# Kernel optimization log

Hardware: AMD Instinct MI355X
Metric: run time of the kernel (lower is better)

## Reference

```python
import jax, jax.numpy as jnp
import numpy as np

B, L, D, E, F, K = 2, 1024, 768, 16, 3072, 2


def setup_inputs() -> dict:
    key = jax.random.key(0)
    ks = jax.random.split(key, 6)
    s = 0.02  # GPT-style init scale
    x = jax.random.normal(ks[0], (B, L, D), dtype=jnp.float32)
    wr = jax.random.normal(ks[1], (E, D), dtype=jnp.float32) * s   # router.weight [out,in]
    w1 = jax.random.normal(ks[2], (E, F, D), dtype=jnp.float32) * s  # expert fc1 weights
    b1 = jnp.zeros((E, F), dtype=jnp.float32)
    w2 = jax.random.normal(ks[3], (E, D, F), dtype=jnp.float32) * s  # expert fc2 weights
    b2 = jnp.zeros((E, D), dtype=jnp.float32)
    return {"x": x, "wr": wr, "w1": w1, "b1": b1, "w2": w2, "b2": b2}


def reference(x, wr, w1, b1, w2, b2):
    # --- router: softmax over experts, top-k gate built by scatter ---
    logits = jnp.einsum("bld,ed->ble", x, wr)            # [B,L,E]
    probs = jax.nn.softmax(logits, axis=-1)
    top_p, ix = jax.lax.top_k(probs, K)                   # [B,L,K]
    # gate[b,l,e] = top_p where e in ix else 0  (scatter_ equivalent)
    gate = jnp.sum(jax.nn.one_hot(ix, E, dtype=x.dtype) * top_p[..., None], axis=-2)  # [B,L,E]
    # --- dense: every expert over every token (matches original loop) ---
    h = jnp.einsum("bld,efd->blef", x, w1) + b1           # [B,L,E,F]
    h = jax.nn.gelu(h, approximate=False)                 # torch nn.GELU (exact erf)
    y = jnp.einsum("blef,edf->bled", h, w2) + b2          # [B,L,E,D]
    out = x + jnp.einsum("bled,ble->bld", y, gate)        # gated combine + residual
    return out
```

## Files before the change

kernel.cpp:

```cpp
#include <hip/hip_runtime.h>


#define D_      768
#define E_      16
#define F_      3072
#define NTOK    2048
#define NROWS   4096
#define SEG     384
#define MAXROWS 6144
#define BK      64
#define BNW     192

typedef __attribute__((ext_vector_type(2))) unsigned int   u32x2;
typedef __attribute__((ext_vector_type(4))) unsigned int   u32x4;
typedef __attribute__((ext_vector_type(8))) unsigned short u16x8;
typedef __attribute__((ext_vector_type(8))) short          v8bf;
typedef __attribute__((ext_vector_type(4))) float          f32x4;

static __device__ inline unsigned short f2bf(float f) {
    unsigned u = __builtin_bit_cast(unsigned, f);
    u += 0x7fffu + ((u >> 16) & 1u);
    return (unsigned short)(u >> 16);
}
static __device__ __forceinline__ unsigned cvt_pk_bf16(float lo, float hi) {
    unsigned r;
    asm("v_cvt_pk_bf16_f32 %0, %1, %2" : "=v"(r) : "v"(lo), "v"(hi));
    return r;
}

__global__ void router_kernel(const float* __restrict__ x, const float* __restrict__ wr,
                              int* __restrict__ idx, float* __restrict__ gate) {
    const int tok  = blockIdx.x;
    const int lane = threadIdx.x;
    const float* xr = x + (size_t)tok * D_;

    float xv[12];
#pragma unroll
    for (int j = 0; j < 12; ++j) xv[j] = xr[lane + 64 * j];

    float lg[E_];
#pragma unroll
    for (int e = 0; e < E_; ++e) {
        const float* w = wr + (size_t)e * D_;
        float acc = 0.f;
#pragma unroll
        for (int j = 0; j < 12; ++j) acc += xv[j] * w[lane + 64 * j];
#pragma unroll
        for (int s = 32; s > 0; s >>= 1) acc += __shfl_xor(acc, s, 64);
        lg[e] = acc;
    }

    float m = lg[0];
#pragma unroll
    for (int e = 1; e < E_; ++e) m = fmaxf(m, lg[e]);
    float p[E_], s = 0.f;
#pragma unroll
    for (int e = 0; e < E_; ++e) { p[e] = expf(lg[e] - m); s += p[e]; }
    const float inv = 1.f / s;

    int e0 = 0; float p0 = p[0];
#pragma unroll
    for (int e = 1; e < E_; ++e) if (p[e] > p0) { p0 = p[e]; e0 = e; }
    int e1 = -1; float p1 = -1.f;
#pragma unroll
    for (int e = 0; e < E_; ++e) if (e != e0 && p[e] > p1) { p1 = p[e]; e1 = e; }

    if (lane == 0) {
        idx[tok * 2 + 0] = e0;  gate[tok * 2 + 0] = p0 * inv;
        idx[tok * 2 + 1] = e1;  gate[tok * 2 + 1] = p1 * inv;
    }
}

__global__ void build_kernel(const int* __restrict__ idx, const float* __restrict__ gate,
                             int* __restrict__ rowmap, float* __restrict__ rowgate,
                             int* __restrict__ posOf) {
    __shared__ int cur[E_];
    const int t = threadIdx.x;
    if (t < E_) cur[t] = 0;
    __syncthreads();
    for (int i = t; i < MAXROWS; i += 256) { rowmap[i] = 0; rowgate[i] = 0.f; }
    __syncthreads();
    for (int i = t; i < NROWS; i += 256) {
        const int e = idx[i];
        const int o = atomicAdd(&cur[e], 1);
        if (o < SEG) {
            const int pos = e * SEG + o;
            rowmap[pos]  = i >> 1;
            rowgate[pos] = gate[i];
            posOf[i]     = pos;
        } else {
            posOf[i] = e * SEG;
        }
    }
}

__global__ void gather_kernel(const float* __restrict__ x, const int* __restrict__ rowmap,
                              unsigned short* __restrict__ Xg) {
    const int g = blockIdx.x * 256 + threadIdx.x;
    const int pos = g / (D_ / 8), c = g % (D_ / 8);
    const int tok = rowmap[pos];
    const float* src = x + (size_t)tok * D_ + c * 8;
    f32x4 a = *(const f32x4*)src;
    f32x4 b = *(const f32x4*)(src + 4);
    u16x8 o;
    o[0] = f2bf(a[0]); o[1] = f2bf(a[1]); o[2] = f2bf(a[2]); o[3] = f2bf(a[3]);
    o[4] = f2bf(b[0]); o[5] = f2bf(b[1]); o[6] = f2bf(b[2]); o[7] = f2bf(b[3]);
    *(u16x8*)(Xg + (size_t)pos * D_ + c * 8) = o;
}

template <int EPI, int NNSH, int KLEN>
__global__ __launch_bounds__(1024, 4)
void gemm_kernel(const unsigned short* __restrict__ Ag, const float* __restrict__ Bw,
                 const float* __restrict__ bias, unsigned short* __restrict__ C0,
                 unsigned short* __restrict__ C123, const float* __restrict__ rowgate,
                 const int K, const int N) {
    constexpr int NT = KLEN / BK;

    const int bid   = blockIdx.x;
    const int e     = bid & 15;
    const int rest  = bid >> 4;
    const int n     = rest & ((1 << NNSH) - 1);
    const int split = rest >> NNSH;
    const int m0    = e * SEG;
    const int n0    = n * BNW;
    const int kOff  = split * KLEN;

    __shared__ alignas(16) unsigned short As[2][SEG * BK];
    __shared__ alignas(16) unsigned short Bs[2][BNW * BK];

    const int t    = threadIdx.x;
    const int lane = t & 63;
    const int wv   = t >> 6;
    const int wm   = wv >> 2;
    const int wn   = wv & 3;
    const int r16  = lane & 15;
    const int h    = lane >> 4;
    const int xorL = (r16 & 7) << 4;

    f32x4 acc[6][3];
#pragma unroll
    for (int i = 0; i < 6; ++i)
#pragma unroll
        for (int j = 0; j < 3; ++j) acc[i][j] = (f32x4){0.f, 0.f, 0.f, 0.f};

    unsigned aByte[3];  int aPhys[3];
#pragma unroll
    for (int i = 0; i < 3; ++i) {
        const int c = t + 1024 * i, r = c >> 3, s = c & 7;
        aByte[i] = (unsigned)(((m0 + r) * K + kOff + s * 8) * 2);
        aPhys[i] = r * 64 + ((s ^ (r & 7)) * 8);
    }
    unsigned bByte[3];  int bOff[3];
#pragma unroll
    for (int i = 0; i < 3; ++i) {
        const int sB = t + 1024 * i, r = sB >> 4, c = sB & 15;
        bByte[i] = (unsigned)((((e * N) + n0 + r) * (size_t)K + kOff + c * 4) * 4);
        bOff[i]  = r * 64 + ((((c >> 1) ^ (r & 7))) << 3) + (c & 1) * 4;
    }

    u32x4 areg[3];
    f32x4 breg[3];

    auto loadA = [&](int kt) {
#pragma unroll
        for (int i = 0; i < 3; ++i)
            areg[i] = *(const u32x4*)((const char*)Ag + aByte[i] + kt * (BK * 2));
    };
    auto loadB = [&](int kt) {
#pragma unroll
        for (int i = 0; i < 3; ++i)
            breg[i] = *(const f32x4*)((const char*)Bw + bByte[i] + kt * (BK * 4));
    };
    auto writeA = [&](int buf) {
#pragma unroll
        for (int i = 0; i < 3; ++i)
            *(u32x4*)&As[buf][aPhys[i]] = areg[i];
    };
    auto writeB = [&](int buf) {
#pragma unroll
        for (int i = 0; i < 3; ++i) {
            u32x2 q;
            q[0] = cvt_pk_bf16(breg[i][0], breg[i][1]);
            q[1] = cvt_pk_bf16(breg[i][2], breg[i][3]);
            *(u32x2*)&Bs[buf][bOff[i]] = q;
        }
    };
    auto compute = [&](int buf) {
#pragma unroll
        for (int ks = 0; ks < 2; ++ks) {
            const int co = ((ks * 64 + h * 16) ^ xorL) >> 1;
            v8bf bfr[3];
#pragma unroll
            for (int nf = 0; nf < 3; ++nf)
                bfr[nf] = *(const v8bf*)&Bs[buf][(wn * 48 + nf * 16 + r16) * 64 + co];
#pragma unroll
            for (int mf = 0; mf < 6; ++mf) {
                const v8bf af = *(const v8bf*)&As[buf][(wm * 96 + mf * 16 + r16) * 64 + co];
#pragma unroll
                for (int nf = 0; nf < 3; ++nf)
                    acc[mf][nf] = __builtin_amdgcn_mfma_f32_16x16x32_bf16(
                        af, bfr[nf], acc[mf][nf], 0, 0, 0);
            }
        }
    };

    loadA(0); loadB(0);
    writeB(0); writeA(0);
    __syncthreads();

    int cb = 0;
    for (int kt = 0; kt < NT; ++kt) {
        if (kt + 1 < NT) { loadB(kt + 1); loadA(kt + 1); }
        compute(cb);
        if (kt + 1 < NT) { writeB(cb ^ 1); writeA(cb ^ 1); }
        __syncthreads();
        cb ^= 1;
    }

    unsigned short* myC = (EPI == 0 || split == 0)
                        ? C0 : C123 + (size_t)(split - 1) * MAXROWS * N;
#pragma unroll
    for (int mf = 0; mf < 6; ++mf) {
#pragma unroll
        for (int jj = 0; jj < 4; ++jj) {
            const int rr = m0 + wm * 96 + mf * 16 + h * 4 + jj;
            float gt = 0.f;
            if (EPI == 1) gt = rowgate[rr];
#pragma unroll
            for (int nf = 0; nf < 3; ++nf) {
                const int cc = n0 + wn * 48 + nf * 16 + r16;
                float v = acc[mf][nf][jj];
                if (EPI == 0) {
                    v += bias[e * N + cc];
                    const float ge = 0.5f * v * (1.f + erff(v * 0.70710678118654752f));
                    myC[(size_t)rr * N + cc] = f2bf(ge);
                } else {
                    if (split == 0) v += bias[e * N + cc];
                    myC[(size_t)rr * N + cc] = f2bf(v * gt);
                }
            }
        }
    }
}

__global__ void combine_kernel(const float* __restrict__ x,
                               const unsigned short* __restrict__ Yp0,
                               const unsigned short* __restrict__ Yp123,
                               const int* __restrict__ posOf, float* __restrict__ out,
                               const int nsplit) {
    const int tok = blockIdx.x;
    const int t   = threadIdx.x;
    const int p0 = posOf[tok * 2 + 0];
    const int p1 = posOf[tok * 2 + 1];
    f32x4 v = *(const f32x4*)(x + (size_t)tok * D_ + t * 4);
    for (int s = 0; s < nsplit; ++s) {
        const unsigned short* base = (s == 0) ? Yp0
                                   : Yp123 + (size_t)(s - 1) * MAXROWS * D_;
        const unsigned short* a = base + (size_t)p0 * D_ + t * 4;
        const unsigned short* b = base + (size_t)p1 * D_ + t * 4;
#pragma unroll
        for (int i = 0; i < 4; ++i) {
            v[i] += __builtin_bit_cast(float, (unsigned)a[i] << 16);
            v[i] += __builtin_bit_cast(float, (unsigned)b[i] << 16);
        }
    }
    *(f32x4*)(out + (size_t)tok * D_ + t * 4) = v;
}

extern "C" void kernel_launch(void* const* d_in, const int* in_sizes, int n_in,
                              void* d_out, int out_size, void* d_ws, size_t ws_size,
                              hipStream_t stream) {
    const float* x  = (const float*)d_in[0];
    const float* wr = (const float*)d_in[1];
    const float* w1 = (const float*)d_in[2];
    const float* b1 = (const float*)d_in[3];
    const float* w2 = (const float*)d_in[4];
    const float* b2 = (const float*)d_in[5];
    float* out = (float*)d_out;

    char* wsp = (char*)d_ws;
    int*            idxP    = (int*)(wsp + 0);
    float*          gateP   = (float*)(wsp + 16384);
    int*            posOf   = (int*)(wsp + 32768);
    int*            rowmap  = (int*)(wsp + 49152);
    float*          rowgate = (float*)(wsp + 73728);
    const size_t    XG_OFF  = 131072;
    const size_t    PLANE   = (size_t)MAXROWS * D_ * 2;
    const size_t    H_OFF   = XG_OFF + PLANE;
    const size_t    H_BYTES = (size_t)MAXROWS * F_ * 2;
    unsigned short* Xg    = (unsigned short*)(wsp + XG_OFF);
    unsigned short* H     = (unsigned short*)(wsp + H_OFF);
    unsigned short* Yp0   = Xg;
    unsigned short* Yp123 = (unsigned short*)(wsp + H_OFF + H_BYTES);

    const bool split4 = (ws_size >= H_OFF + H_BYTES + 3 * PLANE);

    router_kernel<<<NTOK, 64, 0, stream>>>(x, wr, idxP, gateP);
    build_kernel<<<1, 256, 0, stream>>>(idxP, gateP, rowmap, rowgate, posOf);
    gather_kernel<<<MAXROWS * (D_ / 8) / 256, 256, 0, stream>>>(x, rowmap, Xg);

    gemm_kernel<0, 4, 768><<<E_ * 16, 1024, 0, stream>>>(
        Xg, w1, b1, H, (unsigned short*)nullptr, rowgate, D_, F_);

    if (split4) {
        gemm_kernel<1, 2, 768><<<E_ * 16, 1024, 0, stream>>>(
            H, w2, b2, Yp0, Yp123, rowgate, F_, D_);
        combine_kernel<<<NTOK, 192, 0, stream>>>(x, Yp0, Yp123, posOf, out, 4);
    } else {
        gemm_kernel<1, 2, 3072><<<E_ * 4, 1024, 0, stream>>>(
            H, w2, b2, Yp0, Yp123, rowgate, F_, D_);
        combine_kernel<<<NTOK, 192, 0, stream>>>(x, Yp0, Yp123, posOf, out, 1);
    }
}
```

Before: 159.2 us.

## Shrink GEMM tiles and skip MFMA work for unused expert row slabs

Halves the GEMM tile width and K-step, reduces blocks to 512 threads (8 waves), and doubles grid size so more workgroups run concurrently. The build kernel now records per-expert token counts, and waves whose 96-row slab lies beyond the expert's valid rows skip MFMA compute and the epilogue. This aims to avoid wasted matrix work on padded rows of the 384-row expert segments and to improve occupancy, at the cost of more global weight re-reads and more loop iterations with barriers.

```diff
diff --git a/kernel.cpp b/kernel.cpp
--- a/kernel.cpp
+++ b/kernel.cpp
@@ -8,8 +8,8 @@
 #define NROWS   4096
 #define SEG     384
 #define MAXROWS 6144
-#define BK      64
-#define BNW     192
+#define BK      32
+#define BNW     96
 
 typedef __attribute__((ext_vector_type(2))) unsigned int   u32x2;
 typedef __attribute__((ext_vector_type(4))) unsigned int   u32x4;
@@ -73,7 +73,7 @@
 
 __global__ void build_kernel(const int* __restrict__ idx, const float* __restrict__ gate,
                              int* __restrict__ rowmap, float* __restrict__ rowgate,
-                             int* __restrict__ posOf) {
+                             int* __restrict__ posOf, int* __restrict__ meta) {
     __shared__ int cur[E_];
     const int t = threadIdx.x;
     if (t < E_) cur[t] = 0;
@@ -92,6 +92,8 @@
             posOf[i] = e * SEG;
         }
     }
+    __syncthreads();
+    if (t < E_) meta[t] = cur[t] < SEG ? cur[t] : SEG;
 }
 
 __global__ void gather_kernel(const float* __restrict__ x, const int* __restrict__ rowmap,
@@ -109,11 +111,11 @@
 }
 
 template <int EPI, int NNSH, int KLEN>
-__global__ __launch_bounds__(1024, 4)
+__global__ __launch_bounds__(512, 4)
 void gemm_kernel(const unsigned short* __restrict__ Ag, const float* __restrict__ Bw,
                  const float* __restrict__ bias, unsigned short* __restrict__ C0,
                  unsigned short* __restrict__ C123, const float* __restrict__ rowgate,
-                 const int K, const int N) {
+                 const int* __restrict__ meta, const int K, const int N) {
     constexpr int NT = KLEN / BK;
 
     const int bid   = blockIdx.x;
@@ -131,11 +133,14 @@
     const int t    = threadIdx.x;
     const int lane = t & 63;
     const int wv   = t >> 6;
-    const int wm   = wv >> 2;
-    const int wn   = wv & 3;
+    const int wm   = wv >> 1;
+    const int wn   = wv & 1;
     const int r16  = lane & 15;
     const int h    = lane >> 4;
-    const int xorL = (r16 & 7) << 4;
+    const int co   = ((h ^ ((r16 >> 1) & 3)) * 8);
+
+    const int  cnt = meta[e];
+    const bool act = (wm * 96) < cnt;
 
     f32x4 acc[6][3];
 #pragma unroll
@@ -146,20 +151,22 @@
     unsigned aByte[3];  int aPhys[3];
 #pragma unroll
     for (int i = 0; i < 3; ++i) {
-        const int c = t + 1024 * i, r = c >> 3, s = c & 7;
+        const int c = t + 512 * i, r = c >> 2, s = c & 3;
         aByte[i] = (unsigned)(((m0 + r) * K + kOff + s * 8) * 2);
-        aPhys[i] = r * 64 + ((s ^ (r & 7)) * 8);
-    }
-    unsigned bByte[3];  int bOff[3];
-#pragma unroll
-    for (int i = 0; i < 3; ++i) {
-        const int sB = t + 1024 * i, r = sB >> 4, c = sB & 15;
+        aPhys[i] = r * 32 + ((s ^ ((r >> 1) & 3)) * 8);
+    }
+    unsigned bByte[2];  int bOff[2];
+#pragma unroll
+    for (int i = 0; i < 2; ++i) {
+        const int sB = t + 512 * i;
+        const int r = sB >> 3, c = sB & 7;
         bByte[i] = (unsigned)((((e * N) + n0 + r) * (size_t)K + kOff + c * 4) * 4);
-        bOff[i]  = r * 64 + ((((c >> 1) ^ (r & 7))) << 3) + (c & 1) * 4;
-    }
+        bOff[i]  = r * 32 + ((((c >> 1) ^ ((r >> 1) & 3))) * 8) + (c & 1) * 4;
+    }
+    const bool b2 = (t < 256);
 
     u32x4 areg[3];
-    f32x4 breg[3];
+    f32x4 breg[2];
 
     auto loadA = [&](int kt) {
 #pragma unroll
@@ -167,9 +174,8 @@
             areg[i] = *(const u32x4*)((const char*)Ag + aByte[i] + kt * (BK * 2));
     };
     auto loadB = [&](int kt) {
-#pragma unroll
-        for (int i = 0; i < 3; ++i)
-            breg[i] = *(const f32x4*)((const char*)Bw + bByte[i] + kt * (BK * 4));
+        breg[0] = *(const f32x4*)((const char*)Bw + bByte[0] + kt * (BK * 4));
+        if (b2) breg[1] = *(const f32x4*)((const char*)Bw + bByte[1] + kt * (BK * 4));
     };
     auto writeA = [&](int buf) {
 #pragma unroll
@@ -177,46 +183,46 @@
             *(u32x4*)&As[buf][aPhys[i]] = areg[i];
     };
     auto writeB = [&](int buf) {
-#pragma unroll
-        for (int i = 0; i < 3; ++i) {
-            u32x2 q;
-            q[0] = cvt_pk_bf16(breg[i][0], breg[i][1]);
-            q[1] = cvt_pk_bf16(breg[i][2], breg[i][3]);
-            *(u32x2*)&Bs[buf][bOff[i]] = q;
+        u32x2 q;
+        q[0] = cvt_pk_bf16(breg[0][0], breg[0][1]);
+        q[1] = cvt_pk_bf16(breg[0][2], breg[0][3]);
+        *(u32x2*)&Bs[buf][bOff[0]] = q;
+        if (b2) {
+            q[0] = cvt_pk_bf16(breg[1][0], breg[1][1]);
+            q[1] = cvt_pk_bf16(breg[1][2], breg[1][3]);
+            *(u32x2*)&Bs[buf][bOff[1]] = q;
         }
     };
     auto compute = [&](int buf) {
-#pragma unroll
-        for (int ks = 0; ks < 2; ++ks) {
-            const int co = ((ks * 64 + h * 16) ^ xorL) >> 1;
-            v8bf bfr[3];
+        if (!act) return;
+        v8bf bfr[3];
+#pragma unroll
+        for (int nf = 0; nf < 3; ++nf)
+            bfr[nf] = *(const v8bf*)&Bs[buf][(wn * 48 + nf * 16 + r16) * 32 + co];
+#pragma unroll
+        for (int mf = 0; mf < 6; ++mf) {
+            const v8bf af = *(const v8bf*)&As[buf][(wm * 96 + mf * 16 + r16) * 32 + co];
 #pragma unroll
             for (int nf = 0; nf < 3; ++nf)
-                bfr[nf] = *(const v8bf*)&Bs[buf][(wn * 48 + nf * 16 + r16) * 64 + co];
-#pragma unroll
-            for (int mf = 0; mf < 6; ++mf) {
-                const v8bf af = *(const v8bf*)&As[buf][(wm * 96 + mf * 16 + r16) * 64 + co];
-#pragma unroll
-                for (int nf = 0; nf < 3; ++nf)
-                    acc[mf][nf] = __builtin_amdgcn_mfma_f32_16x16x32_bf16(
-                        af, bfr[nf], acc[mf][nf], 0, 0, 0);
-            }
+                acc[mf][nf] = __builtin_amdgcn_mfma_f32_16x16x32_bf16(
+                    af, bfr[nf], acc[mf][nf], 0, 0, 0);
         }
     };
 
     loadA(0); loadB(0);
-    writeB(0); writeA(0);
+    writeA(0); writeB(0);
     __syncthreads();
 
     int cb = 0;
     for (int kt = 0; kt < NT; ++kt) {
         if (kt + 1 < NT) { loadB(kt + 1); loadA(kt + 1); }
         compute(cb);
-        if (kt + 1 < NT) { writeB(cb ^ 1); writeA(cb ^ 1); }
+        if (kt + 1 < NT) { writeA(cb ^ 1); writeB(cb ^ 1); }
         __syncthreads();
         cb ^= 1;
     }
 
+    if (!act) return;
     unsigned short* myC = (EPI == 0 || split == 0)
                         ? C0 : C123 + (size_t)(split - 1) * MAXROWS * N;
 #pragma unroll
@@ -284,6 +290,7 @@
     int*            posOf   = (int*)(wsp + 32768);
     int*            rowmap  = (int*)(wsp + 49152);
     float*          rowgate = (float*)(wsp + 73728);
+    int*            meta    = (int*)(wsp + 98304);
     const size_t    XG_OFF  = 131072;
     const size_t    PLANE   = (size_t)MAXROWS * D_ * 2;
     const size_t    H_OFF   = XG_OFF + PLANE;
@@ -296,19 +303,19 @@
     const bool split4 = (ws_size >= H_OFF + H_BYTES + 3 * PLANE);
 
     router_kernel<<<NTOK, 64, 0, stream>>>(x, wr, idxP, gateP);
-    build_kernel<<<1, 256, 0, stream>>>(idxP, gateP, rowmap, rowgate, posOf);
+    build_kernel<<<1, 256, 0, stream>>>(idxP, gateP, rowmap, rowgate, posOf, meta);
     gather_kernel<<<MAXROWS * (D_ / 8) / 256, 256, 0, stream>>>(x, rowmap, Xg);
 
-    gemm_kernel<0, 4, 768><<<E_ * 16, 1024, 0, stream>>>(
-        Xg, w1, b1, H, (unsigned short*)nullptr, rowgate, D_, F_);
+    gemm_kernel<0, 5, 768><<<E_ * 32, 512, 0, stream>>>(
+        Xg, w1, b1, H, (unsigned short*)nullptr, rowgate, meta, D_, F_);
 
     if (split4) {
-        gemm_kernel<1, 2, 768><<<E_ * 16, 1024, 0, stream>>>(
-            H, w2, b2, Yp0, Yp123, rowgate, F_, D_);
+        gemm_kernel<1, 3, 768><<<E_ * 8 * 4, 512, 0, stream>>>(
+            H, w2, b2, Yp0, Yp123, rowgate, meta, F_, D_);
         combine_kernel<<<NTOK, 192, 0, stream>>>(x, Yp0, Yp123, posOf, out, 4);
     } else {
-        gemm_kernel<1, 2, 3072><<<E_ * 4, 1024, 0, stream>>>(
-            H, w2, b2, Yp0, Yp123, rowgate, F_, D_);
+        gemm_kernel<1, 3, 3072><<<E_ * 8, 512, 0, stream>>>(
+            H, w2, b2, Yp0, Yp123, rowgate, meta, F_, D_);
         combine_kernel<<<NTOK, 192, 0, stream>>>(x, Yp0, Yp123, posOf, out, 1);
     }
 }
```

New measurement: 323.2 us. 103% more time.
